# Optimization experiments

Hardware: AMD Instinct MI355X
Metric: run time of the kernel (lower is better)

The kernel has to match this reference:

```python
import jax, jax.numpy as jnp
import numpy as np

B, S, D, MULT, K, EPS = 8, 2048, 512, 4, 9, 1e-6


def setup_inputs() -> dict:
    key = jax.random.key(0)
    ks = jax.random.split(key, 12)
    w = lambda k, shape, s=0.02: jax.random.normal(k, shape, dtype=jnp.float32) * s
    return dict(
        x=jax.random.normal(ks[0], (B, S, D), dtype=jnp.float32),
        g=jnp.ones((D,), jnp.float32),
        W1=w(ks[1], (D, D)), b1=jnp.zeros((D,), jnp.float32),
        W2=w(ks[2], (D, D)), b2=jnp.zeros((D,), jnp.float32),
        dw_w=w(ks[3], (D, D, K)), dw_b=jnp.zeros((D,), jnp.float32),
        pw_w=w(ks[4], (D, D, 1)), pw_b=jnp.zeros((D,), jnp.float32),
        Wi=w(ks[5], (D, D)), bi=jnp.zeros((D,), jnp.float32),
        Wr=w(ks[6], (D, D)), br=jnp.zeros((D,), jnp.float32),
        lam=jax.random.normal(ks[7], (D,), dtype=jnp.float32),
        Wm1=w(ks[8], (D, D * MULT)), bm1=jnp.zeros((D * MULT,), jnp.float32),
        Wm2=w(ks[9], (D * MULT, D)), bm2=jnp.zeros((D,), jnp.float32),
    )


def _rglru(x, Wi, bi, Wr, br, lam):
    # Griffin RG-LRU: h_t = a_t * h_{t-1} + sqrt(1 - a_t^2) * (i_t * x_t), h_0 = 0
    r = jax.nn.sigmoid(x @ Wr + br)                 # [B,S,D] recurrence gate
    i = jax.nn.sigmoid(x @ Wi + bi)                 # [B,S,D] input gate
    log_a = -8.0 * jax.nn.softplus(lam) * r         # [B,S,D]
    a = jnp.exp(log_a)
    b = jnp.sqrt(1.0 - jnp.exp(2.0 * log_a)) * (i * x)

    def combine(e1, e2):
        a1, b1 = e1
        a2, b2 = e2
        return (a1 * a2, a2 * b1 + b2)

    _, h = jax.lax.associative_scan(combine, (a, b), axis=1)
    return h


def _conv1d(x_cdS, w_oik, b_o, pad):
    y = jax.lax.conv_general_dilated(
        x_cdS, w_oik, window_strides=(1,), padding=[pad],
        dimension_numbers=("NCH", "OIH", "NCH"))
    return y + b_o[None, :, None]


def reference(x, g, W1, b1, W2, b2, dw_w, dw_b, pw_w, pw_b,
              Wi, bi, Wr, br, lam, Wm1, bm1, Wm2, bm2):
    scale = jnp.sqrt(jnp.float32(D))

    def rms(t):  # matches torch: x / (||x||_2 + eps) * sqrt(D) * g
        n = jnp.linalg.norm(t, axis=-1, keepdims=True) + EPS
        return t / n * scale * g

    skip = x
    xn = rms(x)
    l1 = xn @ W1 + b1                               # [B,S,D]
    l2 = xn @ W2 + b2                               # [B,S,D]
    c = jnp.transpose(l1, (0, 2, 1))                # [B,D,S]
    c = _conv1d(c, dw_w, dw_b, (K // 2, K // 2))    # 'same' padding, k=9
    c = _conv1d(c, pw_w, pw_b, (0, 0))              # pointwise k=1
    l1 = jnp.transpose(c, (0, 2, 1))                # [B,S,D]
    l1 = _rglru(l1, Wi, bi, Wr, br, lam)
    x1 = l1 * jax.nn.gelu(l2, approximate=False) + skip

    skip2 = x1
    xn2 = rms(x1)
    h = xn2 @ Wm1 + bm1                             # [B,S,4D]
    out = (jax.nn.gelu(h, approximate=False) * h) @ Wm2 + bm2 + skip2
    return out
```

## Files before the change

kernel.cpp:

```cpp
#include <hip/hip_runtime.h>
#include <hip/hip_bf16.h>

typedef unsigned short ushort_t;
typedef unsigned short vus8 __attribute__((ext_vector_type(8)));
typedef short vs8 __attribute__((ext_vector_type(8)));
typedef float vf4 __attribute__((ext_vector_type(4)));

#define D_DIM 512
#define S_LEN 2048
#define B_SZ 8
#define T_TOK 16384
#define NCH 64
#define CLEN 32

__device__ __forceinline__ float bf2f(ushort_t u) {
  union { unsigned int i; float f; } v;
  v.i = ((unsigned int)u) << 16;
  return v.f;
}
__device__ __forceinline__ ushort_t f2bf(float f) {
  union { float f; unsigned int i; } v;
  v.f = f;
  unsigned int r = v.i + 0x7fffu + ((v.i >> 16) & 1u);
  return (ushort_t)(r >> 16);
}
__device__ __forceinline__ float gelu_exact(float x) {
  return 0.5f * x * (1.0f + erff(x * 0.7071067811865475f));
}
__device__ __forceinline__ float ld_in(const void* p, size_t i, int fl) {
  return fl ? ((const float*)p)[i] : bf2f(((const ushort_t*)p)[i]);
}
__device__ __forceinline__ int dt_fl(const ushort_t* gdt) {
  return !(gdt[0] == 0x3F80 && gdt[1] == 0x3F80);
}
__device__ __forceinline__ void gld_lds16(const ushort_t* g, ushort_t* l) {
  __builtin_amdgcn_global_load_lds(
      (const __attribute__((address_space(1))) unsigned int*)g,
      (__attribute__((address_space(3))) unsigned int*)l, 16, 0, 0);
}

__device__ __forceinline__ void ab_compute(ushort_t rp, ushort_t ip, ushort_t xv,
                                           float sp8, float& a, float& b) {
  float r = 1.f / (1.f + expf(-bf2f(rp)));
  float ig = 1.f / (1.f + expf(-bf2f(ip)));
  float la = -sp8 * r;
  a = expf(la);
  b = sqrtf(fmaxf(0.f, -expm1f(2.f * la))) * ig * bf2f(xv);
}

#define NJOBS 18
struct PrepJobs {
  const void* src[NJOBS];
  ushort_t* dst[NJOBS];
  int R[NJOBS];
  int C[NJOBS];
  int mode[NJOBS];
  int start[NJOBS];
  const void* gsrc;
  int njobs;
};
__global__ void mega_prep(PrepJobs J, const ushort_t* __restrict__ gdt) {
  __shared__ ushort_t ts[32][33];
  int fl = dt_fl(gdt);
  int bid = blockIdx.x;
  int j = 0;
  while (j + 1 < J.njobs && bid >= J.start[j + 1]) j++;
  int tile = bid - J.start[j];
  const void* in = J.src[j];
  ushort_t* out = J.dst[j];
  int mode = J.mode[j];
  if (mode == 2) {
    int n = J.R[j];
    int base = tile * 8192;
#pragma unroll 4
    for (int q = 0; q < 32; q++) {
      int i = base + q * 256 + threadIdx.x;
      if (i < n) out[i] = fl ? f2bf(((const float*)in)[i]) : ((const ushort_t*)in)[i];
    }
    return;
  }
  int R = J.R[j], C = J.C[j];
  int tpr = C >> 5;
  int bc = tile % tpr, br = tile / tpr;
  int tx = threadIdx.x & 31, ty = threadIdx.x >> 5;
#pragma unroll
  for (int i = 0; i < 32; i += 8) {
    size_t idx = (size_t)(br * 32 + ty + i) * C + bc * 32 + tx;
    ts[ty + i][tx] = fl ? f2bf(((const float*)in)[idx]) : ((const ushort_t*)in)[idx];
  }
  __syncthreads();
#pragma unroll
  for (int i = 0; i < 32; i += 8) {
    int r = bc * 32 + ty + i;
    int orow = (mode == 1) ? (r % 9) * 512 + r / 9 : r;
    ushort_t val = ts[tx][ty + i];
    if (mode == 3) {
      int kcol = br * 32 + tx;
      val = f2bf(bf2f(val) * ld_in(J.gsrc, kcol, fl));
    }
    out[(size_t)orow * R + br * 32 + tx] = val;
  }
}

__global__ void gam_kernel(const ushort_t* __restrict__ tpw, const ushort_t* __restrict__ dwbc,
                           const ushort_t* __restrict__ pwbc, const ushort_t* __restrict__ lamc,
                           float* __restrict__ gam, float* __restrict__ sp8b) {
  int t = blockIdx.x * 256 + threadIdx.x;
  if (t < 512) {
    float l = bf2f(lamc[t]);
    sp8b[t] = 8.f * ((l > 20.f) ? l : log1pf(expf(l)));
  }
  int wave = threadIdx.x >> 6, lane = threadIdx.x & 63;
  int o = blockIdx.x * 4 + wave;
  vus8 v = *(const vus8*)(tpw + (size_t)o * 512 + lane * 8);
  vus8 w = *(const vus8*)(dwbc + lane * 8);
  float p = 0.f;
#pragma unroll
  for (int q = 0; q < 8; q++) p += bf2f(v[q]) * bf2f(w[q]);
#pragma unroll
  for (int off = 32; off; off >>= 1) p += __shfl_xor(p, off, 64);
  if (lane == 0) gam[o] = p + bf2f(pwbc[o]);
}

__global__ void rms_kernel(const void* __restrict__ x, const ushort_t* __restrict__ gdt,
                           const ushort_t* __restrict__ gc, ushort_t* __restrict__ out) {
  int fl = dt_fl(gdt);
  int wave = threadIdx.x >> 6, lane = threadIdx.x & 63;
  int row = blockIdx.x * 4 + wave;
  size_t base = (size_t)row * D_DIM + lane * 8;
  float f[8];
  float ss = 0.f;
#pragma unroll
  for (int j = 0; j < 8; j++) { f[j] = ld_in(x, base + j, fl); ss += f[j] * f[j]; }
#pragma unroll
  for (int off = 32; off > 0; off >>= 1) ss += __shfl_xor(ss, off, 64);
  float sc = 22.62741699796952f / (sqrtf(ss) + 1e-6f);
  vus8 o;
#pragma unroll
  for (int j = 0; j < 8; j++) o[j] = f2bf(f[j] * sc * bf2f(gc[lane * 8 + j]));
  *(vus8*)(out + base) = o;
}

template <int ACT>
__global__ __launch_bounds__(256, 2) void gemm_bt(
    const ushort_t* __restrict__ A, const ushort_t* __restrict__ Bt,
    const ushort_t* __restrict__ bias, void* __restrict__ Cv,
    const ushort_t* __restrict__ skip, const float* __restrict__ rowss,
    const ushort_t* __restrict__ gdt, int N, int K, int lda, int row0,
    size_t zsA, size_t zsB, size_t zsC) {
  __shared__ __align__(16) ushort_t As[128 * 32];
  __shared__ __align__(16) ushort_t Bs[128 * 32];
  A += (size_t)blockIdx.z * zsA;
  Bt += (size_t)blockIdx.z * zsB;
  const size_t zC = (size_t)blockIdx.z * zsC;
  const int tid = threadIdx.x;
  const int bm = blockIdx.y, bn = blockIdx.x;
  const int wave = tid >> 6, lane = tid & 63;
  const int wm = wave & 1, wn = wave >> 1;
  const int quad = lane >> 4, l16 = lane & 15;
  const int ofl = (ACT == 2) ? dt_fl(gdt) : 0;
  const int srow = wave * 32 + (lane >> 2);
  const int scol = (lane & 3) * 8;
  const ushort_t* gA = A + (size_t)(bm * 128 + srow) * lda + scol;
  const ushort_t* gB = Bt + (size_t)(bn * 128 + srow) * K + scol;
  ushort_t* lA0 = As + (wave * 32) * 32;
  ushort_t* lA1 = As + (wave * 32 + 16) * 32;
  ushort_t* lB0 = Bs + (wave * 32) * 32;
  ushort_t* lB1 = Bs + (wave * 32 + 16) * 32;
  vf4 acc[4][4] = {};
  for (int k0 = 0; k0 < K; k0 += 32) {
    __syncthreads();
    gld_lds16(gA + k0, lA0);
    gld_lds16(gA + k0 + (size_t)16 * lda, lA1);
    gld_lds16(gB + k0, lB0);
    gld_lds16(gB + k0 + (size_t)16 * K, lB1);
    __syncthreads();
    vs8 af[4], bfr[4];
#pragma unroll
    for (int mi = 0; mi < 4; mi++)
      af[mi] = *(const vs8*)(As + (wm * 64 + mi * 16 + l16) * 32 + quad * 8);
#pragma unroll
    for (int ni = 0; ni < 4; ni++)
      bfr[ni] = *(const vs8*)(Bs + (wn * 64 + ni * 16 + l16) * 32 + quad * 8);
#pragma unroll
    for (int mi = 0; mi < 4; mi++)
#pragma unroll
      for (int ni = 0; ni < 4; ni++)
        acc[mi][ni] =
            __builtin_amdgcn_mfma_f32_16x16x32_bf16(af[mi], bfr[ni], acc[mi][ni], 0, 0, 0);
  }
#pragma unroll
  for (int mi = 0; mi < 4; mi++) {
#pragma unroll
    for (int ni = 0; ni < 4; ni++) {
      int gcol = bn * 128 + wn * 64 + ni * 16 + l16;
      float bv = bias ? bf2f(bias[gcol]) : 0.f;
#pragma unroll
      for (int r = 0; r < 4; r++) {
        int grow = row0 + bm * 128 + wm * 64 + mi * 16 + quad * 4 + r;
        size_t oidx = zC + (size_t)grow * N + gcol;
        float v;
        if (ACT == 3) {
          float sc = 22.62741699796952f / (sqrtf(rowss[grow]) + 1e-6f);
          v = acc[mi][ni][r] * sc + bv;
          v = gelu_exact(v) * v;
        } else {
          v = acc[mi][ni][r] + bv;
        }
        if (ACT == 2) v += bf2f(skip[(size_t)grow * N + gcol]);
        if (ACT == 2 && ofl) ((float*)Cv)[oidx] = v;
        else ((ushort_t*)Cv)[oidx] = f2bf(v);
      }
    }
  }
}

#define LDA_CONV 1024
__global__ __launch_bounds__(256, 2) void conv_gemm(
    const ushort_t* __restrict__ A, const ushort_t* __restrict__ Bt9,
    const float* __restrict__ gam, ushort_t* __restrict__ C) {
  __shared__ __align__(16) ushort_t Ah[136 * 32];
  __shared__ __align__(16) ushort_t Bs[3 * 128 * 32];
  const int tid = threadIdx.x;
  const int bid = blockIdx.x;
  const int xid = bid & 7, cid = bid >> 3;
  const int bn = xid >> 1;
  const int bm = (xid & 1) * 64 + cid;
  const int wave = tid >> 6, lane = tid & 63;
  const int wm = wave & 1, wn = wave >> 1;
  const int quad = lane >> 4, l16 = lane & 15;
  const int pos = bm & 15;
  const bool first = (pos == 0), last = (pos == 15);
  const int blrow = lane >> 2;
  const int bscol = (lane & 3) * 8;
  vf4 acc[4][4] = {};
  for (int k0 = 0; k0 < D_DIM; k0 += 32) {
    __syncthreads();
    for (int c = tid; c < 544; c += 256) {
      int j = c >> 2, col = (c & 3) * 8;
      vus8 v = {0, 0, 0, 0, 0, 0, 0, 0};
      bool valid = !((first && j < 4) || (last && j >= 132));
      if (valid)
        v = *(const vus8*)(A + (size_t)(bm * 128 + j - 4) * LDA_CONV + k0 + col);
      *(vus8*)(Ah + j * 32 + col) = v;
    }
#pragma unroll
    for (int kg = 0; kg < 3; kg++) {
      if (kg) __syncthreads();
#pragma unroll
      for (int h = 0; h < 6; h++) {
        int m = h * 4 + wave;
        int r = m * 16 + blrow;
        int kbl = m >> 3;
        int ro = r & 127;
        const ushort_t* g = Bt9 + ((size_t)(kg * 3 + kbl) * D_DIM + bn * 128 + ro) * D_DIM +
                            k0 + bscol;
        gld_lds16(g, Bs + m * 16 * 32);
      }
      __syncthreads();
#pragma unroll
      for (int kbl = 0; kbl < 3; kbl++) {
        int kb = kg * 3 + kbl;
        vs8 af[4], bfr[4];
#pragma unroll
        for (int mi = 0; mi < 4; mi++)
          af[mi] = *(const vs8*)(Ah + (wm * 64 + mi * 16 + l16 + kb) * 32 + quad * 8);
#pragma unroll
        for (int ni = 0; ni < 4; ni++)
          bfr[ni] = *(const vs8*)(Bs + kbl * 4096 + (wn * 64 + ni * 16 + l16) * 32 + quad * 8);
#pragma unroll
        for (int mi = 0; mi < 4; mi++)
#pragma unroll
          for (int ni = 0; ni < 4; ni++)
            acc[mi][ni] =
                __builtin_amdgcn_mfma_f32_16x16x32_bf16(af[mi], bfr[ni], acc[mi][ni], 0, 0, 0);
      }
    }
  }
#pragma unroll
  for (int mi = 0; mi < 4; mi++) {
#pragma unroll
    for (int ni = 0; ni < 4; ni++) {
      int gcol = bn * 128 + wn * 64 + ni * 16 + l16;
      float gv = gam[gcol];
#pragma unroll
      for (int r = 0; r < 4; r++) {
        int grow = bm * 128 + wm * 64 + mi * 16 + quad * 4 + r;
        C[(size_t)grow * D_DIM + gcol] = f2bf(acc[mi][ni][r] + gv);
      }
    }
  }
}

__global__ void scan_pass1(const ushort_t* __restrict__ P, const ushort_t* __restrict__ xin,
                           const float* __restrict__ sp8b, float* __restrict__ Aagg,
                           float* __restrict__ Bagg) {
  int bid = blockIdx.x;
  int dblk = bid & 1, c = (bid >> 1) & (NCH - 1), bb = bid >> 7;
  int d = dblk * 256 + threadIdx.x;
  float sp8 = sp8b[d];
  size_t baseP = ((size_t)bb * S_LEN + c * CLEN) * 1024 + d;
  size_t baseX = ((size_t)bb * S_LEN + c * CLEN) * D_DIM + d;
  float Ap = 1.f, h = 0.f;
  for (int s = 0; s < CLEN; s++) {
    float av, bv;
    ab_compute(P[baseP + (size_t)s * 1024], P[baseP + 512 + (size_t)s * 1024],
               xin[baseX + (size_t)s * D_DIM], sp8, av, bv);
    Ap *= av;
    h = av * h + bv;
  }
  size_t o = ((size_t)bb * NCH + c) * D_DIM + d;
  Aagg[o] = Ap;
  Bagg[o] = h;
}

__global__ void scan_carry(const float* __restrict__ Aagg, const float* __restrict__ Bagg,
                           float* __restrict__ carry) {
  int idx = blockIdx.x * 256 + threadIdx.x;
  int bb = idx >> 9, d = idx & (D_DIM - 1);
  float h = 0.f;
  for (int c = 0; c < NCH; c++) {
    size_t o = ((size_t)bb * NCH + c) * D_DIM + d;
    carry[o] = h;
    h = Aagg[o] * h + Bagg[o];
  }
}

__global__ void scan_pass2(const ushort_t* __restrict__ P, const float* __restrict__ sp8b,
                           const float* __restrict__ carry, const ushort_t* __restrict__ P12,
                           const void* __restrict__ x, const ushort_t* __restrict__ gdt,
                           ushort_t* xio, float* __restrict__ rowss) {
  int fl = dt_fl(gdt);
  int bid = blockIdx.x;
  int dblk = bid & 1, c = (bid >> 1) & (NCH - 1), bb = bid >> 7;
  int d = dblk * 256 + threadIdx.x;
  int lane = threadIdx.x & 63;
  float sp8 = sp8b[d];
  float h = carry[((size_t)bb * NCH + c) * D_DIM + d];
  size_t baseP = ((size_t)bb * S_LEN + c * CLEN) * 1024 + d;
  size_t baseL = ((size_t)bb * S_LEN + c * CLEN) * 1024 + 512 + d;
  size_t base = ((size_t)bb * S_LEN + c * CLEN) * D_DIM + d;
  int row0 = bb * S_LEN + c * CLEN;
  for (int s = 0; s < CLEN; s++) {
    size_t idx = base + (size_t)s * D_DIM;
    float av, bv;
    ab_compute(P[baseP + (size_t)s * 1024], P[baseP + 512 + (size_t)s * 1024], xio[idx], sp8,
               av, bv);
    h = av * h + bv;
    float l2v = bf2f(P12[baseL + (size_t)s * 1024]);
    float xv = ld_in(x, idx, fl);
    float v = h * gelu_exact(l2v) + xv;
    xio[idx] = f2bf(v);
    float p = v * v;
#pragma unroll
    for (int o2 = 32; o2; o2 >>= 1) p += __shfl_xor(p, o2, 64);
    if (lane == 0) atomicAdd(&rowss[row0 + s], p);
  }
}

extern "C" void kernel_launch(void* const* d_in, const int* in_sizes, int n_in, void* d_out,
                              int out_size, void* d_ws, size_t ws_size, hipStream_t stream) {
  (void)in_sizes; (void)n_in; (void)out_size; (void)ws_size;
  const void* x   = d_in[0];
  const void* g   = d_in[1];
  const void* W1  = d_in[2];
  const void* b1  = d_in[3];
  const void* W2  = d_in[4];
  const void* b2  = d_in[5];
  const void* dww = d_in[6];
  const void* dwb = d_in[7];
  const void* pww = d_in[8];
  const void* pwb = d_in[9];
  const void* Wi  = d_in[10];
  const void* bi  = d_in[11];
  const void* Wr  = d_in[12];
  const void* br  = d_in[13];
  const void* lam = d_in[14];
  const void* Wm1 = d_in[15];
  const void* bm1 = d_in[16];
  const void* Wm2 = d_in[17];
  const void* bm2 = d_in[18];
  const ushort_t* gdt = (const ushort_t*)g;

  char* ws = (char*)d_ws;
  size_t off = 0;
  auto take = [&](size_t n) {
    void* p = ws + off;
    off += (n + 255) & ~(size_t)255;
    return p;
  };
  const size_t ACT_B = (size_t)T_TOK * D_DIM * 2;
  ushort_t* tW12 = (ushort_t*)take((size_t)1024 * 512 * 2);
  ushort_t* tWri = (ushort_t*)take((size_t)1024 * 512 * 2);
  ushort_t* tWm1 = (ushort_t*)take((size_t)2048 * 512 * 2);
  ushort_t* tWm2 = (ushort_t*)take((size_t)2048 * 512 * 2);
  ushort_t* Wp   = (ushort_t*)take((size_t)9 * 512 * 512 * 2);
  ushort_t* gc   = (ushort_t*)take(512 * 2);
  ushort_t* lamc = (ushort_t*)take(512 * 2);
  ushort_t* b12c = (ushort_t*)take(1024 * 2);
  ushort_t* bric = (ushort_t*)take(1024 * 2);
  ushort_t* bm2c = (ushort_t*)take(512 * 2);
  ushort_t* bm1c = (ushort_t*)take(2048 * 2);
  ushort_t* dwbc = (ushort_t*)take(512 * 2);
  ushort_t* pwbc = (ushort_t*)take(512 * 2);
  float* gam     = (float*)take(512 * 4);
  float* sp8b    = (float*)take(512 * 4);
  float* rowss   = (float*)take((size_t)T_TOK * 4);
  ushort_t* S0 = (ushort_t*)take(ACT_B);
  ushort_t* S1 = (ushort_t*)take(ACT_B);
  ushort_t* S2 = (ushort_t*)take(ACT_B);
  ushort_t* S3 = (ushort_t*)take(ACT_B);
  ushort_t* S4 = (ushort_t*)take(ACT_B);
  float* Aagg  = (float*)take((size_t)B_SZ * NCH * D_DIM * 4);
  float* Bagg  = (float*)take((size_t)B_SZ * NCH * D_DIM * 4);
  float* carry = (float*)take((size_t)B_SZ * NCH * D_DIM * 4);
  ushort_t* tpw  = S0;
  ushort_t* tdwT = S1;
  ushort_t* Pri  = S0;
  ushort_t* P12  = S2;
  ushort_t* u    = S0;

  hipMemsetAsync(rowss, 0, (size_t)T_TOK * 4, stream);

  PrepJobs J;
  const void* js[NJOBS] = {g, lam, b1, b2, dwb, pwb, br, bi, bm2, bm1, pww,
                           W1, W2, Wr, Wi, Wm1, Wm2, dww};
  ushort_t* jd[NJOBS] = {gc, lamc, b12c, b12c + 512, dwbc, pwbc, bric, bric + 512, bm2c, bm1c,
                         tpw, tW12, tW12 + (size_t)512 * 512, tWri, tWri + (size_t)512 * 512,
                         tWm1, tWm2, tdwT};
  int jR[NJOBS] = {512, 512, 512, 512, 512, 512, 512, 512, 512, 2048, 262144,
                   512, 512, 512, 512, 512, 2048, 512};
  int jC[NJOBS] = {0, 0, 0, 0, 0, 0, 0, 0, 0, 0, 0, 512, 512, 512, 512, 2048, 512, 4608};
  int jm[NJOBS] = {2, 2, 2, 2, 2, 2, 2, 2, 2, 2, 2, 0, 0, 0, 0, 3, 0, 1};
  int cum = 0;
  for (int i = 0; i < NJOBS; i++) {
    J.src[i] = js[i]; J.dst[i] = jd[i]; J.R[i] = jR[i]; J.C[i] = jC[i]; J.mode[i] = jm[i];
    J.start[i] = cum;
    cum += (jm[i] == 2) ? (jR[i] + 8191) / 8192 : (jC[i] / 32) * (jR[i] / 32);
  }
  J.gsrc = g;
  J.njobs = NJOBS;
  mega_prep<<<cum, 256, 0, stream>>>(J, gdt);
  gemm_bt<0><<<dim3(4, 4, 9), 256, 0, stream>>>(tpw, tdwT, nullptr, Wp, nullptr, nullptr, gdt,
                                                512, 512, 512, 0, 0, (size_t)512 * 512,
                                                (size_t)512 * 512);
  gam_kernel<<<128, 256, 0, stream>>>(tpw, dwbc, pwbc, lamc, gam, sp8b);

  rms_kernel<<<T_TOK / 4, 256, 0, stream>>>(x, gdt, gc, S4);
  gemm_bt<0><<<dim3(8, 128), 256, 0, stream>>>(S4, tW12, b12c, P12, nullptr, nullptr, gdt,
                                               1024, 512, 512, 0, 0, 0, 0);
  conv_gemm<<<512, 256, 0, stream>>>(P12, Wp, gam, S4);
  gemm_bt<0><<<dim3(8, 128), 256, 0, stream>>>(S4, tWri, bric, Pri, nullptr, nullptr, gdt,
                                               1024, 512, 512, 0, 0, 0, 0);
  scan_pass1<<<B_SZ * NCH * 2, 256, 0, stream>>>(Pri, S4, sp8b, Aagg, Bagg);
  scan_carry<<<16, 256, 0, stream>>>(Aagg, Bagg, carry);
  scan_pass2<<<B_SZ * NCH * 2, 256, 0, stream>>>(Pri, sp8b, carry, P12, x, gdt, S4, rowss);

  gemm_bt<3><<<dim3(16, 128), 256, 0, stream>>>(S4, tWm1, bm1c, u, nullptr, rowss, gdt, 2048,
                                                512, 512, 0, 0, 0, 0);
  gemm_bt<2><<<dim3(4, 128), 256, 0, stream>>>(u, tWm2, bm2c, d_out, S4, nullptr, gdt, 512,
                                               2048, 2048, 0, 0, 0, 0);
}
```

Before: 520.2 us.

## Add 256x256-tile 512-thread GEMM kernel and use it for three projections

Introduces a new bf16 MFMA GEMM with 256x256 output tiles, 8 waves, a 4-slot LDS ring prefetching two k-steps ahead via direct global-to-LDS loads, swizzled columns, and raised wave priority around the MFMA block. It replaces the 128x128 gemm_bt for the W1/W2, Wi/Wr and Wm1 projections, aiming to raise arithmetic intensity and cut global/LDS traffic per FLOP. The larger tile uses 128 KB of LDS and many accumulator registers, which lowers occupancy. It also produces fewer blocks, so the grid may fill the GPU's compute units less evenly.

```diff
diff --git a/kernel.cpp b/kernel.cpp
--- a/kernel.cpp
+++ b/kernel.cpp
@@ -210,6 +210,102 @@
         if (ACT == 2) v += bf2f(skip[(size_t)grow * N + gcol]);
         if (ACT == 2 && ofl) ((float*)Cv)[oidx] = v;
         else ((ushort_t*)Cv)[oidx] = f2bf(v);
+      }
+    }
+  }
+}
+
+template <int ACT>
+__global__ __launch_bounds__(512, 2) void gemm256(
+    const ushort_t* __restrict__ A, const ushort_t* __restrict__ Bt,
+    const ushort_t* __restrict__ bias, ushort_t* __restrict__ C,
+    const float* __restrict__ rowss, int N, int K) {
+  __shared__ __align__(16) ushort_t lds[65536];
+  const int tid = threadIdx.x;
+  const int bn = blockIdx.x, bm = blockIdx.y;
+  const int wave = tid >> 6, lane = tid & 63;
+  const int wm = wave & 1, wn = wave >> 1;
+  const int quad = lane >> 4, l16 = lane & 15;
+  const int NT = K >> 5;
+
+  const int r2 = tid >> 2;
+  const int scol = (((tid & 3) ^ ((r2 >> 1) & 3)) << 3);
+  const ushort_t* gA0 = A + (size_t)(bm * 256 + r2) * K + scol;
+  const ushort_t* gB0 = Bt + (size_t)(bn * 256 + r2) * K + scol;
+  const size_t hstep = (size_t)128 * K;
+  ushort_t* ldsW = lds + (wave << 9);
+
+  const int cA = ((quad ^ ((l16 >> 1) & 3)) << 3);
+
+  vf4 acc[8][4] = {};
+
+#define STAGE(t, slot)                            \
+  do {                                            \
+    const ushort_t* ga = gA0 + (t) * 32;          \
+    const ushort_t* gb = gB0 + (t) * 32;          \
+    ushort_t* d = ldsW + (slot) * 16384;          \
+    gld_lds16(ga, d);                             \
+    gld_lds16(ga + hstep, d + 4096);              \
+    gld_lds16(gb, d + 8192);                      \
+    gld_lds16(gb + hstep, d + 12288);             \
+  } while (0)
+
+  STAGE(0, 0);
+  STAGE(1, 1);
+
+  for (int t = 0; t < NT; ++t) {
+    if (t + 1 < NT)
+      asm volatile("s_waitcnt vmcnt(4)" ::: "memory");
+    else
+      asm volatile("s_waitcnt vmcnt(0)" ::: "memory");
+    __builtin_amdgcn_s_barrier();
+    __builtin_amdgcn_sched_barrier(0);
+    if (t + 2 < NT) STAGE(t + 2, (t + 2) & 3);
+    const ushort_t* L = lds + (t & 3) * 16384;
+    vs8 af[8], bf[4];
+#pragma unroll
+    for (int mi = 0; mi < 8; mi++)
+      af[mi] = *(const vs8*)(L + (wm * 128 + mi * 16 + l16) * 32 + cA);
+#pragma unroll
+    for (int ni = 0; ni < 4; ni++)
+      bf[ni] = *(const vs8*)(L + 8192 + (wn * 64 + ni * 16 + l16) * 32 + cA);
+    asm volatile("s_waitcnt lgkmcnt(0)" ::: "memory");
+    __builtin_amdgcn_sched_barrier(0);
+    __builtin_amdgcn_s_setprio(1);
+#pragma unroll
+    for (int mi = 0; mi < 8; mi++)
+#pragma unroll
+      for (int ni = 0; ni < 4; ni++)
+        acc[mi][ni] =
+            __builtin_amdgcn_mfma_f32_16x16x32_bf16(af[mi], bf[ni], acc[mi][ni], 0, 0, 0);
+    __builtin_amdgcn_s_setprio(0);
+    __builtin_amdgcn_sched_barrier(0);
+  }
+#undef STAGE
+
+#pragma unroll
+  for (int mi = 0; mi < 8; mi++) {
+    const int growb = bm * 256 + wm * 128 + mi * 16 + quad * 4;
+    float scv[4];
+    if (ACT == 3) {
+#pragma unroll
+      for (int r = 0; r < 4; r++)
+        scv[r] = 22.62741699796952f / (sqrtf(rowss[growb + r]) + 1e-6f);
+    }
+#pragma unroll
+    for (int ni = 0; ni < 4; ni++) {
+      const int gcol = bn * 256 + wn * 64 + ni * 16 + l16;
+      const float bv = bf2f(bias[gcol]);
+#pragma unroll
+      for (int r = 0; r < 4; r++) {
+        float v = acc[mi][ni][r];
+        if (ACT == 3) {
+          v = v * scv[r] + bv;
+          v = gelu_exact(v) * v;
+        } else {
+          v += bv;
+        }
+        C[(size_t)(growb + r) * N + gcol] = f2bf(v);
       }
     }
   }
@@ -447,17 +543,14 @@
   gam_kernel<<<128, 256, 0, stream>>>(tpw, dwbc, pwbc, lamc, gam, sp8b);
 
   rms_kernel<<<T_TOK / 4, 256, 0, stream>>>(x, gdt, gc, S4);
-  gemm_bt<0><<<dim3(8, 128), 256, 0, stream>>>(S4, tW12, b12c, P12, nullptr, nullptr, gdt,
-                                               1024, 512, 512, 0, 0, 0, 0);
+  gemm256<0><<<dim3(4, 64), 512, 0, stream>>>(S4, tW12, b12c, P12, nullptr, 1024, 512);
   conv_gemm<<<512, 256, 0, stream>>>(P12, Wp, gam, S4);
-  gemm_bt<0><<<dim3(8, 128), 256, 0, stream>>>(S4, tWri, bric, Pri, nullptr, nullptr, gdt,
-                                               1024, 512, 512, 0, 0, 0, 0);
+  gemm256<0><<<dim3(4, 64), 512, 0, stream>>>(S4, tWri, bric, Pri, nullptr, 1024, 512);
   scan_pass1<<<B_SZ * NCH * 2, 256, 0, stream>>>(Pri, S4, sp8b, Aagg, Bagg);
   scan_carry<<<16, 256, 0, stream>>>(Aagg, Bagg, carry);
   scan_pass2<<<B_SZ * NCH * 2, 256, 0, stream>>>(Pri, sp8b, carry, P12, x, gdt, S4, rowss);
 
-  gemm_bt<3><<<dim3(16, 128), 256, 0, stream>>>(S4, tWm1, bm1c, u, nullptr, rowss, gdt, 2048,
-                                                512, 512, 0, 0, 0, 0);
+  gemm256<3><<<dim3(8, 64), 512, 0, stream>>>(S4, tWm1, bm1c, u, rowss, 2048, 512);
   gemm_bt<2><<<dim3(4, 128), 256, 0, stream>>>(u, tWm2, bm2c, d_out, S4, nullptr, gdt, 512,
                                                2048, 2048, 0, 0, 0, 0);
 }
```

New measurement: 509.5 us. -2.0%, faster.
